# Optimization experiments

Hardware: AMD Instinct MI355X
Metric: run time of the kernel (lower is better)

Reference implementation:

```python
import jax, jax.numpy as jnp
import numpy as np

TOP_K = 8


def setup_inputs() -> dict:
    key = jax.random.key(0)
    k1, k2 = jax.random.split(key)
    B, S, D, E = 4, 4096, 2048, 64
    x = jax.random.normal(k1, (B, S, D), dtype=jnp.float32)
    # nn.Linear(d_model, n_experts): weight [E, D], bias [E]
    W = jax.random.normal(k2, (E, D), dtype=jnp.float32) * (1.0 / np.sqrt(D))
    b = jnp.zeros((E,), dtype=jnp.float32)
    return {"x": x, "W": W, "b": b}


def reference(x, W, b):
    # logits: [B, S, E] = x @ W^T + b
    logits = jnp.einsum("bsd,ed->bse", x, W) + b
    scores = jax.nn.sigmoid(logits)                      # [B, S, E]
    B, S, E = scores.shape
    flat = scores.reshape(B * S, E)                      # tokens x experts
    top_w, top_idx = jax.lax.top_k(flat, TOP_K)          # [B*S, k]
    return top_w.reshape(B, S, TOP_K), top_idx.reshape(B, S, TOP_K)
```

## Files before the change

kernel.cpp:

```cpp
#include <hip/hip_runtime.h>
#include <math.h>

#define TOKENS 16384
#define DMODEL 2048
#define NEXP   64
#define TOPK   8
#define BM     64
#define BK     32
#define PAD    4

__global__ __launch_bounds__(256) void router_gemm(
    const float* __restrict__ x, const float* __restrict__ W,
    float* __restrict__ part, int kchunk)
{
    __shared__ float xsT[BK][BM + PAD];
    __shared__ float wsT[BK][NEXP + PAD];

    const int tid = threadIdx.x;
    const int kq  = tid & 7;
    const int row = tid >> 3;
    const int ty  = tid >> 4;
    const int tx  = tid & 15;
    const size_t tokBase = (size_t)blockIdx.x * BM;
    const int    kc      = blockIdx.y;
    const size_t kbase   = (size_t)kc * (size_t)kchunk;

    double accd[4][4];
    float  accf[4][4];
#pragma unroll
    for (int i = 0; i < 4; ++i)
#pragma unroll
        for (int j = 0; j < 4; ++j) { accd[i][j] = 0.0; accf[i][j] = 0.0f; }

    const int ntiles = kchunk / BK;

    const float* xp = x + (tokBase + row) * DMODEL + kbase + kq * 4;
    const float* wp = W + (size_t)row * DMODEL + kbase + kq * 4;

    float4 xa = *(const float4*)(xp);
    float4 xb = *(const float4*)(xp + (size_t)32 * DMODEL);
    float4 wa = *(const float4*)(wp);
    float4 wb = *(const float4*)(wp + (size_t)32 * DMODEL);

    for (int t = 0; t < ntiles; ++t) {
        __syncthreads();
        xsT[kq * 4 + 0][row] = xa.x; xsT[kq * 4 + 1][row] = xa.y;
        xsT[kq * 4 + 2][row] = xa.z; xsT[kq * 4 + 3][row] = xa.w;
        xsT[kq * 4 + 0][row + 32] = xb.x; xsT[kq * 4 + 1][row + 32] = xb.y;
        xsT[kq * 4 + 2][row + 32] = xb.z; xsT[kq * 4 + 3][row + 32] = xb.w;
        wsT[kq * 4 + 0][row] = wa.x; wsT[kq * 4 + 1][row] = wa.y;
        wsT[kq * 4 + 2][row] = wa.z; wsT[kq * 4 + 3][row] = wa.w;
        wsT[kq * 4 + 0][row + 32] = wb.x; wsT[kq * 4 + 1][row + 32] = wb.y;
        wsT[kq * 4 + 2][row + 32] = wb.z; wsT[kq * 4 + 3][row + 32] = wb.w;
        __syncthreads();

        if (t + 1 < ntiles) {
            xp += BK; wp += BK;
            xa = *(const float4*)(xp);
            xb = *(const float4*)(xp + (size_t)32 * DMODEL);
            wa = *(const float4*)(wp);
            wb = *(const float4*)(wp + (size_t)32 * DMODEL);
        }

#pragma unroll
        for (int kk = 0; kk < BK; ++kk) {
            const float4 a = *(const float4*)(&xsT[kk][ty * 4]);
            const float4 b = *(const float4*)(&wsT[kk][tx * 4]);
            const float av[4] = {a.x, a.y, a.z, a.w};
            const float bv[4] = {b.x, b.y, b.z, b.w};
#pragma unroll
            for (int i = 0; i < 4; ++i)
#pragma unroll
                for (int j = 0; j < 4; ++j)
                    accf[i][j] = fmaf(av[i], bv[j], accf[i][j]);
        }
#pragma unroll
        for (int i = 0; i < 4; ++i)
#pragma unroll
            for (int j = 0; j < 4; ++j) {
                accd[i][j] += (double)accf[i][j];
                accf[i][j] = 0.0f;
            }
    }

#pragma unroll
    for (int i = 0; i < 4; ++i) {
        const size_t tok = tokBase + ty * 4 + i;
        float4 o;
        o.x = (float)accd[i][0]; o.y = (float)accd[i][1];
        o.z = (float)accd[i][2]; o.w = (float)accd[i][3];
        *(float4*)(part + ((size_t)kc * TOKENS + tok) * NEXP + tx * 4) = o;
    }
}

__global__ __launch_bounds__(256) void router_reduce_topk(
    const float* __restrict__ part, const float* __restrict__ bias,
    float* __restrict__ out_w, float* __restrict__ out_i, int ksplit)
{
    const int lane = threadIdx.x & 63;
    const int wid  = threadIdx.x >> 6;
    const size_t t = (size_t)blockIdx.x * 4 + wid;

    double vd = (double)bias[lane];
    for (int kc = 0; kc < ksplit; ++kc)
        vd += (double)part[((size_t)kc * TOKENS + t) * NEXP + lane];
    float v = (float)vd;

    const int myi = lane;
    float bv = 0.0f; int bi = 0;
#pragma unroll
    for (int r = 0; r < TOPK; ++r) {
        float mv = v; int mi = myi;
#pragma unroll
        for (int off = 32; off > 0; off >>= 1) {
            const float ov = __shfl_xor(mv, off, 64);
            const int   oi = __shfl_xor(mi, off, 64);
            if (ov > mv || (ov == mv && oi < mi)) { mv = ov; mi = oi; }
        }
        if (lane == r)  { bv = mv; bi = mi; }
        if (myi == mi)  { v = -INFINITY; }
    }

    if (lane < TOPK) {
        out_w[t * TOPK + lane] = 1.0f / (1.0f + expf(-bv));
        out_i[t * TOPK + lane] = (float)bi;
    }
}

extern "C" void kernel_launch(void* const* d_in, const int* in_sizes, int n_in,
                              void* d_out, int out_size, void* d_ws, size_t ws_size,
                              hipStream_t stream) {
    const float* x    = (const float*)d_in[0];
    const float* W    = (const float*)d_in[1];
    const float* bias = (const float*)d_in[2];
    float* out_w = (float*)d_out;
    float* out_i = (float*)d_out + (size_t)TOKENS * TOPK;
    float* part  = (float*)d_ws;

    const size_t per = (size_t)TOKENS * NEXP * sizeof(float);
    int ksplit = 8;
    while (ksplit > 1 && ws_size < (size_t)ksplit * per) ksplit >>= 1;
    const int kchunk = DMODEL / ksplit;

    dim3 grid(TOKENS / BM, ksplit);
    router_gemm<<<grid, 256, 0, stream>>>(x, W, part, kchunk);
    router_reduce_topk<<<TOKENS / 4, 256, 0, stream>>>(part, bias, out_w, out_i, ksplit);
}
```

Baseline: 232.3 us.

## Use split-bf16 MFMA GEMM fused with top-k, dropping split-K partials

Replaces the scalar FP32 split-K GEMM and separate reduce/top-k kernel with one fused kernel. It splits x and W each into three bf16 parts and runs six bf16 MFMA products per tile to approximate FP32 accuracy. W is pre-converted into a padded bf16 tile image and streamed into LDS with global_load_lds double buffering, and top-k runs directly on logits held in shared memory. This removes the partial-sum workspace round trip and the second launch, at the cost of a small W conversion kernel, extra MFMA work per tile, and possible precision differences that could change near-tied top-k selections.

```diff
diff --git a/kernel.cpp b/kernel.cpp
--- a/kernel.cpp
+++ b/kernel.cpp
@@ -5,125 +5,194 @@
 #define DMODEL 2048
 #define NEXP   64
 #define TOPK   8
-#define BM     64
-#define BK     32
-#define PAD    4
-
-__global__ __launch_bounds__(256) void router_gemm(
-    const float* __restrict__ x, const float* __restrict__ W,
-    float* __restrict__ part, int kchunk)
+#define BM     32
+#define BK     64
+#define NCHUNK (DMODEL / BK)
+#define ROWU   72
+#define WTILEU (NEXP * ROWU)
+#define WT3PAD 14336
+
+typedef unsigned short u16;
+typedef float f32x4 __attribute__((ext_vector_type(4)));
+typedef short s16x8 __attribute__((ext_vector_type(8)));
+
+__device__ __forceinline__ u16 f2bf(float f, float& back) {
+    unsigned u = __float_as_uint(f);
+    unsigned r = u + 0x7fffu + ((u >> 16) & 1u);
+    back = __uint_as_float(r & 0xffff0000u);
+    return (u16)(r >> 16);
+}
+
+__device__ __forceinline__ void gload_lds16(const void* g, void* l) {
+    __builtin_amdgcn_global_load_lds(
+        (const __attribute__((address_space(1))) unsigned int*)g,
+        (__attribute__((address_space(3))) unsigned int*)l, 16, 0, 0);
+}
+
+__global__ __launch_bounds__(256) void wconv(
+    const float* __restrict__ W, u16* __restrict__ wimg)
 {
-    __shared__ float xsT[BK][BM + PAD];
-    __shared__ float wsT[BK][NEXP + PAD];
-
-    const int tid = threadIdx.x;
-    const int kq  = tid & 7;
-    const int row = tid >> 3;
-    const int ty  = tid >> 4;
-    const int tx  = tid & 15;
+    const int id = blockIdx.x * 256 + threadIdx.x;
+    const int e = id >> 11;
+    const int k = id & 2047;
+    const float x = W[id];
+    float f1, f2, fd;
+    const u16 a = f2bf(x, f1);
+    const float d1 = x - f1;
+    const u16 b = f2bf(d1, f2);
+    const float d2 = d1 - f2;
+    const u16 c = f2bf(d2, fd);
+    u16* base = wimg + (size_t)(k >> 6) * WT3PAD + e * ROWU + (k & 63);
+    base[0]          = a;
+    base[WTILEU]     = b;
+    base[2 * WTILEU] = c;
+}
+
+__global__ __launch_bounds__(256) void router_fused(
+    const float* __restrict__ x, const u16* __restrict__ wimg,
+    const float* __restrict__ bias, float* __restrict__ out_w,
+    float* __restrict__ out_i)
+{
+    __shared__ __align__(16) u16 xs[3][BM * ROWU];
+    __shared__ __align__(16) u16 wsb[2][WT3PAD];
+    __shared__ float lg[BM][NEXP + 4];
+
+    const int tid  = threadIdx.x;
+    const int lane = tid & 63;
+    const int w    = tid >> 6;
+    const int wr   = w >> 1;
+    const int wc   = w & 1;
     const size_t tokBase = (size_t)blockIdx.x * BM;
-    const int    kc      = blockIdx.y;
-    const size_t kbase   = (size_t)kc * (size_t)kchunk;
-
-    double accd[4][4];
-    float  accf[4][4];
-#pragma unroll
-    for (int i = 0; i < 4; ++i)
-#pragma unroll
-        for (int j = 0; j < 4; ++j) { accd[i][j] = 0.0; accf[i][j] = 0.0f; }
-
-    const int ntiles = kchunk / BK;
-
-    const float* xp = x + (tokBase + row) * DMODEL + kbase + kq * 4;
-    const float* wp = W + (size_t)row * DMODEL + kbase + kq * 4;
+
+    const int srow = tid >> 3;
+    const int soct = tid & 7;
+    const float* xp = x + (tokBase + srow) * DMODEL + soct * 8;
+
+    const int arow  = wr * 16 + (lane & 15);
+    const int kq    = (lane >> 4) * 8;
+    const int brow0 = wc * 32 + (lane & 15);
+
+    f32x4  acc[2][2];
+    double accd[2][4];
+#pragma unroll
+    for (int i = 0; i < 2; ++i)
+#pragma unroll
+        for (int j = 0; j < 2; ++j)
+            acc[i][j] = (f32x4){0.f, 0.f, 0.f, 0.f};
+#pragma unroll
+    for (int j = 0; j < 2; ++j)
+#pragma unroll
+        for (int r = 0; r < 4; ++r) accd[j][r] = 0.0;
+
+    const char* wgbase = (const char*)wimg;
+#define WCOPY(tt, buf)                                                        \
+    {                                                                         \
+        const char* gsrc_ = wgbase + (size_t)(tt) * (WT3PAD * 2) + w * 1024 + \
+                            lane * 16;                                        \
+        char* ldst_ = (char*)&wsb[buf][0] + w * 1024;                         \
+        _Pragma("unroll") for (int r_ = 0; r_ < 7; ++r_)                      \
+            gload_lds16(gsrc_ + r_ * 4096, ldst_ + r_ * 4096);                \
+    }
 
     float4 xa = *(const float4*)(xp);
-    float4 xb = *(const float4*)(xp + (size_t)32 * DMODEL);
-    float4 wa = *(const float4*)(wp);
-    float4 wb = *(const float4*)(wp + (size_t)32 * DMODEL);
-
-    for (int t = 0; t < ntiles; ++t) {
+    float4 xb = *(const float4*)(xp + 4);
+    WCOPY(0, 0);
+
+    for (int t = 0; t < NCHUNK; ++t) {
         __syncthreads();
-        xsT[kq * 4 + 0][row] = xa.x; xsT[kq * 4 + 1][row] = xa.y;
-        xsT[kq * 4 + 2][row] = xa.z; xsT[kq * 4 + 3][row] = xa.w;
-        xsT[kq * 4 + 0][row + 32] = xb.x; xsT[kq * 4 + 1][row + 32] = xb.y;
-        xsT[kq * 4 + 2][row + 32] = xb.z; xsT[kq * 4 + 3][row + 32] = xb.w;
-        wsT[kq * 4 + 0][row] = wa.x; wsT[kq * 4 + 1][row] = wa.y;
-        wsT[kq * 4 + 2][row] = wa.z; wsT[kq * 4 + 3][row] = wa.w;
-        wsT[kq * 4 + 0][row + 32] = wb.x; wsT[kq * 4 + 1][row + 32] = wb.y;
-        wsT[kq * 4 + 2][row + 32] = wb.z; wsT[kq * 4 + 3][row + 32] = wb.w;
+        {
+            float xv[8] = {xa.x, xa.y, xa.z, xa.w, xb.x, xb.y, xb.z, xb.w};
+            s16x8 va, vb, vc;
+#pragma unroll
+            for (int j = 0; j < 8; ++j) {
+                float f1, f2, fd;
+                const u16 a1 = f2bf(xv[j], f1);
+                const float d1 = xv[j] - f1;
+                const u16 a2 = f2bf(d1, f2);
+                const float d2 = d1 - f2;
+                const u16 a3 = f2bf(d2, fd);
+                va[j] = (short)a1; vb[j] = (short)a2; vc[j] = (short)a3;
+            }
+            const int ub = srow * ROWU + soct * 8;
+            *(s16x8*)&xs[0][ub] = va;
+            *(s16x8*)&xs[1][ub] = vb;
+            *(s16x8*)&xs[2][ub] = vc;
+        }
         __syncthreads();
-
-        if (t + 1 < ntiles) {
-            xp += BK; wp += BK;
+        if (t + 1 < NCHUNK) {
+            xp += BK;
             xa = *(const float4*)(xp);
-            xb = *(const float4*)(xp + (size_t)32 * DMODEL);
-            wa = *(const float4*)(wp);
-            wb = *(const float4*)(wp + (size_t)32 * DMODEL);
-        }
-
-#pragma unroll
-        for (int kk = 0; kk < BK; ++kk) {
-            const float4 a = *(const float4*)(&xsT[kk][ty * 4]);
-            const float4 b = *(const float4*)(&wsT[kk][tx * 4]);
-            const float av[4] = {a.x, a.y, a.z, a.w};
-            const float bv[4] = {b.x, b.y, b.z, b.w};
-#pragma unroll
-            for (int i = 0; i < 4; ++i)
-#pragma unroll
-                for (int j = 0; j < 4; ++j)
-                    accf[i][j] = fmaf(av[i], bv[j], accf[i][j]);
-        }
-#pragma unroll
-        for (int i = 0; i < 4; ++i)
-#pragma unroll
-            for (int j = 0; j < 4; ++j) {
-                accd[i][j] += (double)accf[i][j];
-                accf[i][j] = 0.0f;
+            xb = *(const float4*)(xp + 4);
+            WCOPY(t + 1, (t + 1) & 1);
+        }
+
+        const u16* wb = &wsb[t & 1][0];
+#pragma unroll
+        for (int ks = 0; ks < 2; ++ks) {
+            const int ko = ks * 32 + kq;
+            const s16x8 a1 = *(const s16x8*)&xs[0][arow * ROWU + ko];
+            const s16x8 a2 = *(const s16x8*)&xs[1][arow * ROWU + ko];
+            const s16x8 a3 = *(const s16x8*)&xs[2][arow * ROWU + ko];
+#pragma unroll
+            for (int nt = 0; nt < 2; ++nt) {
+                const int br = (brow0 + nt * 16) * ROWU + ko;
+                const s16x8 b1 = *(const s16x8*)&wb[0 * WTILEU + br];
+                const s16x8 b2 = *(const s16x8*)&wb[1 * WTILEU + br];
+                const s16x8 b3 = *(const s16x8*)&wb[2 * WTILEU + br];
+                f32x4 t0 = acc[ks][nt];
+                t0 = __builtin_amdgcn_mfma_f32_16x16x32_bf16(a1, b1, t0, 0, 0, 0);
+                t0 = __builtin_amdgcn_mfma_f32_16x16x32_bf16(a1, b2, t0, 0, 0, 0);
+                t0 = __builtin_amdgcn_mfma_f32_16x16x32_bf16(a2, b1, t0, 0, 0, 0);
+                t0 = __builtin_amdgcn_mfma_f32_16x16x32_bf16(a1, b3, t0, 0, 0, 0);
+                t0 = __builtin_amdgcn_mfma_f32_16x16x32_bf16(a3, b1, t0, 0, 0, 0);
+                t0 = __builtin_amdgcn_mfma_f32_16x16x32_bf16(a2, b2, t0, 0, 0, 0);
+                acc[ks][nt] = t0;
+            }
+        }
+#pragma unroll
+        for (int nt = 0; nt < 2; ++nt)
+#pragma unroll
+            for (int r = 0; r < 4; ++r) {
+                accd[nt][r] += (double)acc[0][nt][r] + (double)acc[1][nt][r];
+                acc[0][nt][r] = 0.f;
+                acc[1][nt][r] = 0.f;
             }
     }
 
 #pragma unroll
-    for (int i = 0; i < 4; ++i) {
-        const size_t tok = tokBase + ty * 4 + i;
-        float4 o;
-        o.x = (float)accd[i][0]; o.y = (float)accd[i][1];
-        o.z = (float)accd[i][2]; o.w = (float)accd[i][3];
-        *(float4*)(part + ((size_t)kc * TOKENS + tok) * NEXP + tx * 4) = o;
-    }
-}
-
-__global__ __launch_bounds__(256) void router_reduce_topk(
-    const float* __restrict__ part, const float* __restrict__ bias,
-    float* __restrict__ out_w, float* __restrict__ out_i, int ksplit)
-{
-    const int lane = threadIdx.x & 63;
-    const int wid  = threadIdx.x >> 6;
-    const size_t t = (size_t)blockIdx.x * 4 + wid;
-
-    double vd = (double)bias[lane];
-    for (int kc = 0; kc < ksplit; ++kc)
-        vd += (double)part[((size_t)kc * TOKENS + t) * NEXP + lane];
-    float v = (float)vd;
-
-    const int myi = lane;
-    float bv = 0.0f; int bi = 0;
-#pragma unroll
-    for (int r = 0; r < TOPK; ++r) {
-        float mv = v; int mi = myi;
-#pragma unroll
-        for (int off = 32; off > 0; off >>= 1) {
-            const float ov = __shfl_xor(mv, off, 64);
-            const int   oi = __shfl_xor(mi, off, 64);
-            if (ov > mv || (ov == mv && oi < mi)) { mv = ov; mi = oi; }
-        }
-        if (lane == r)  { bv = mv; bi = mi; }
-        if (myi == mi)  { v = -INFINITY; }
-    }
-
-    if (lane < TOPK) {
-        out_w[t * TOPK + lane] = 1.0f / (1.0f + expf(-bv));
-        out_i[t * TOPK + lane] = (float)bi;
+    for (int nt = 0; nt < 2; ++nt)
+#pragma unroll
+        for (int r = 0; r < 4; ++r) {
+            const int row = wr * 16 + (lane >> 4) * 4 + r;
+            const int col = wc * 32 + nt * 16 + (lane & 15);
+            lg[row][col] = (float)accd[nt][r];
+        }
+    __syncthreads();
+
+    const float be = bias[lane];
+#pragma unroll
+    for (int i = 0; i < 8; ++i) {
+        const int tl = w * 8 + i;
+        float v = lg[tl][lane] + be;
+        const int myi = lane;
+        float bv = 0.0f; int bi = 0;
+#pragma unroll
+        for (int r = 0; r < TOPK; ++r) {
+            float mv = v; int mi = myi;
+#pragma unroll
+            for (int off = 32; off > 0; off >>= 1) {
+                const float ov = __shfl_xor(mv, off, 64);
+                const int   oi = __shfl_xor(mi, off, 64);
+                if (ov > mv || (ov == mv && oi < mi)) { mv = ov; mi = oi; }
+            }
+            if (lane == r) { bv = mv; bi = mi; }
+            if (myi == mi) { v = -INFINITY; }
+        }
+        if (lane < TOPK) {
+            const size_t tok = tokBase + tl;
+            out_w[tok * TOPK + lane] = 1.0f / (1.0f + expf(-bv));
+            out_i[tok * TOPK + lane] = (float)bi;
+        }
     }
 }
 
@@ -135,14 +204,8 @@
     const float* bias = (const float*)d_in[2];
     float* out_w = (float*)d_out;
     float* out_i = (float*)d_out + (size_t)TOKENS * TOPK;
-    float* part  = (float*)d_ws;
-
-    const size_t per = (size_t)TOKENS * NEXP * sizeof(float);
-    int ksplit = 8;
-    while (ksplit > 1 && ws_size < (size_t)ksplit * per) ksplit >>= 1;
-    const int kchunk = DMODEL / ksplit;
-
-    dim3 grid(TOKENS / BM, ksplit);
-    router_gemm<<<grid, 256, 0, stream>>>(x, W, part, kchunk);
-    router_reduce_topk<<<TOKENS / 4, 256, 0, stream>>>(part, bias, out_w, out_i, ksplit);
-}
+    u16* wimg = (u16*)d_ws;
+
+    wconv<<<dim3((NEXP * DMODEL) / 256), 256, 0, stream>>>(W, wimg);
+    router_fused<<<dim3(TOKENS / BM), 256, 0, stream>>>(x, wimg, bias, out_w, out_i);
+}
```

New measurement: 259.4 us. 1.12x slower.
